# Kernel tuning notes

Measured on AMD Instinct MI355X. Metric: run time of the kernel, lower is better.

Reference implementation:

```python
import jax, jax.numpy as jnp
import numpy as np

S, B, I, H = 2048, 64, 128, 128
E = float(np.e)


def setup_inputs() -> dict:
    key = jax.random.key(0)
    ks = jax.random.split(key, 16)
    s = 1.0 / np.sqrt(H)
    inp = {
        "x": jax.random.normal(ks[0], (S, B, I), jnp.float32),
        "h0": jnp.zeros((2, B, H), jnp.float32),
        "c0": jnp.zeros((2, B, H), jnp.float32),
        # elapsed times, strictly positive
        "delta_ts": jax.random.uniform(ks[1], (B, S), jnp.float32, 0.1, 10.0),
    }
    names = ["W_ih", "W_hh", "b_ih", "b_hh", "W_d", "b_d"]
    shapes = [(4 * H, I), (4 * H, H), (4 * H,), (4 * H,), (H, H), (H,)]
    idx = 2
    for d in ["f", "r"]:
        for n, sh in zip(names, shapes):
            inp[f"{n}_{d}"] = jax.random.uniform(ks[idx], sh, jnp.float32, -s, s)
            idx += 1
    return inp


def _run_dir(x, dt, h, c, W_ih, W_hh, b_ih, b_hh, W_d, b_d):
    """Scan a TLSTM cell over time. x: [S,B,I], dt: [S,B]."""
    def step(carry, inp):
        h, c = carry
        xt, dtt = inp
        # time-aware memory decomposition (Baytas et al.)
        c_s = jnp.tanh(c @ W_d.T + b_d)               # short-term memory
        c_adj = c - c_s + c_s / jnp.log(E + dtt[:, None])  # discounted by elapsed time
        gates = xt @ W_ih.T + b_ih + h @ W_hh.T + b_hh
        i_g, f_g, g_g, o_g = jnp.split(gates, 4, axis=-1)
        c_n = jax.nn.sigmoid(f_g) * c_adj + jax.nn.sigmoid(i_g) * jnp.tanh(g_g)
        h_n = jax.nn.sigmoid(o_g) * jnp.tanh(c_n)
        return (h_n, c_n), h_n

    (h, c), ys = jax.lax.scan(step, (h, c), (x, dt))
    return ys, h, c


def reference(x, h0, c0, delta_ts,
              W_ih_f, W_hh_f, b_ih_f, b_hh_f, W_d_f, b_d_f,
              W_ih_r, W_hh_r, b_ih_r, b_hh_r, W_d_r, b_d_r):
    dt = delta_ts.T  # [S, B]
    out_f, _, _ = _run_dir(x, dt, h0[0], c0[0],
                           W_ih_f, W_hh_f, b_ih_f, b_hh_f, W_d_f, b_d_f)
    out_r, _, _ = _run_dir(x[::-1], dt[::-1], h0[1], c0[1],
                           W_ih_r, W_hh_r, b_ih_r, b_hh_r, W_d_r, b_d_r)
    return jnp.concatenate([out_f, out_r[::-1]], axis=-1)  # [S, B, 2H]
```

## Files before the change

kernel.cpp:

```cpp
#include <hip/hip_runtime.h>
#include <hip/hip_bf16.h>

#define SEQ  2048
#define BAT  64
#define HID  128
#define LDSP 136

#define XB_OFF  (1u << 20)
#define IL_OFF  (35u << 20)

typedef __bf16 bf16x8 __attribute__((ext_vector_type(8)));
typedef float  f32x4  __attribute__((ext_vector_type(4)));

#define MFMA(a,b,c) __builtin_amdgcn_mfma_f32_16x16x32_bf16((a),(b),(c),0,0,0)

__device__ __forceinline__ float sig_f(float x) {
    return __fdividef(1.0f, 1.0f + __expf(-x));
}
__device__ __forceinline__ float tanh_f(float x) {
    return 1.0f - __fdividef(2.0f, 1.0f + __expf(2.0f * x));
}
__device__ __forceinline__ bf16x8 cvt8(const float* p) {
    bf16x8 r;
    #pragma unroll
    for (int i = 0; i < 8; ++i) r[i] = (__bf16)p[i];
    return r;
}

__global__ void cvt_x_kernel(const float* __restrict__ x, __bf16* __restrict__ xb) {
    const int i = (blockIdx.x * 256 + threadIdx.x) * 4;
    const float4 v = *reinterpret_cast<const float4*>(x + i);
    __bf16 o[4];
    o[0] = (__bf16)v.x; o[1] = (__bf16)v.y; o[2] = (__bf16)v.z; o[3] = (__bf16)v.w;
    *reinterpret_cast<uint2*>(xb + i) = *reinterpret_cast<const uint2*>(o);
}

__global__ void prep_ilog_kernel(const float* __restrict__ dts, float* __restrict__ il) {
    const int idx = blockIdx.x * 256 + threadIdx.x;
    const int b = idx >> 11, t = idx & 2047;
    const float l = __logf(2.718281828459045f + dts[idx]);
    il[t * BAT + b] = __fdividef(1.0f, l) - 1.0f;
}

__global__ __launch_bounds__(512, 2) void tlstm_main(
    const __bf16* __restrict__ xb,   const float* __restrict__ ilg,
    const float* __restrict__ h0,    const float* __restrict__ c0,
    const float* __restrict__ Wih_f, const float* __restrict__ Whh_f,
    const float* __restrict__ bih_f, const float* __restrict__ bhh_f,
    const float* __restrict__ Wd_f,  const float* __restrict__ bd_f,
    const float* __restrict__ Wih_r, const float* __restrict__ Whh_r,
    const float* __restrict__ bih_r, const float* __restrict__ bhh_r,
    const float* __restrict__ Wd_r,  const float* __restrict__ bd_r,
    float* __restrict__ out)
{
    const int d    = blockIdx.x >> 4;
    const int b0   = (blockIdx.x & 15) * 4;
    const int tid  = threadIdx.x;
    const int w    = tid >> 6;
    const int lane = tid & 63;
    const int nl   = lane & 15;
    const int q    = lane >> 4;
    const int j    = w * 16 + nl;

    const float* Wih = d ? Wih_r : Wih_f;
    const float* Whh = d ? Whh_r : Whh_f;
    const float* bih = d ? bih_r : bih_f;
    const float* bhh = d ? bhh_r : bhh_f;
    const float* Wd  = d ? Wd_r  : Wd_f;
    const float* bd  = d ? bd_r  : bd_f;

    __shared__ __align__(16) __bf16 hc_a[2][16][LDSP];

    bf16x8 whh_fr[4][4], wih_fr[4][4], wd_fr[4];
    #pragma unroll
    for (int g = 0; g < 4; ++g) {
        const int row = g * 128 + j;
        #pragma unroll
        for (int kt = 0; kt < 4; ++kt) {
            const int off = row * HID + kt * 32 + q * 8;
            wih_fr[g][kt] = cvt8(Wih + off);
            whh_fr[g][kt] = cvt8(Whh + off);
        }
    }
    #pragma unroll
    for (int kt = 0; kt < 4; ++kt)
        wd_fr[kt] = cvt8(Wd + j * HID + kt * 32 + q * 8);

    float bias_g[4];
    #pragma unroll
    for (int g = 0; g < 4; ++g)
        bias_g[g] = bih[g * 128 + j] + bhh[g * 128 + j];
    const float bias_d = bd[j];
    const f32x4 bdv = f32x4{bias_d, bias_d, bias_d, bias_d};

    for (int e = tid; e < 4 * HID; e += 512) {
        const int ci = e >> 7, k = e & 127;
        hc_a[0][ci * 4][k]     = (__bf16)h0[(d * BAT + b0 + ci) * HID + k];
        hc_a[0][ci * 4 + 2][k] = (__bf16)c0[(d * BAT + b0 + ci) * HID + k];
    }
    float c_st = c0[(d * BAT + b0 + q) * HID + j];
    __syncthreads();

    const int t0      = d ? (SEQ - 1) : 0;
    const int tstep   = d ? -1 : 1;
    const int xstride = tstep * BAT * HID;
    const int istride = tstep * BAT;
    const int ostride = tstep * BAT * 256;

    const __bf16* xp0 = xb + (size_t)((t0 + tstep * (nl & 3)) * BAT + b0 + (nl >> 2)) * HID + q * 8;
    const float*  ip0 = ilg + (size_t)t0 * BAT + b0 + q;
    float*        op  = out + (size_t)(t0 * BAT + b0 + q) * 256 + d * 128 + j;

    bf16x8 xfrA[4], xfrB[4];
    float  ilA[4], ilB[4];

    #pragma unroll
    for (int kt = 0; kt < 4; ++kt) {
        xfrA[kt] = *reinterpret_cast<const bf16x8*>(xp0 + kt * 32);
        xfrB[kt] = *reinterpret_cast<const bf16x8*>(xp0 + 4 * xstride + kt * 32);
    }
    #pragma unroll
    for (int dtv = 0; dtv < 4; ++dtv) {
        ilA[dtv] = ip0[dtv * istride];
        ilB[dtv] = ip0[(4 + dtv) * istride];
    }
    const __bf16* xpl = xp0 + 8 * xstride;
    const float*  ipl = ip0 + 8 * istride;

    auto chunk = [&](bf16x8 (&xfrCur)[4], float (&ilCur)[4]) __attribute__((always_inline)) {
        f32x4 xacc[4];
        #pragma unroll
        for (int g = 0; g < 4; ++g) {
            const f32x4 bg = f32x4{bias_g[g], bias_g[g], bias_g[g], bias_g[g]};
            xacc[g] = MFMA(xfrCur[0], wih_fr[g][0], bg);
        }
        #pragma unroll
        for (int kt = 1; kt < 4; ++kt) {
            xacc[0] = MFMA(xfrCur[kt], wih_fr[0][kt], xacc[0]);
            xacc[1] = MFMA(xfrCur[kt], wih_fr[1][kt], xacc[1]);
            xacc[2] = MFMA(xfrCur[kt], wih_fr[2][kt], xacc[2]);
            xacc[3] = MFMA(xfrCur[kt], wih_fr[3][kt], xacc[3]);
        }

        #pragma unroll
        for (int dt = 0; dt < 4; ++dt) {
            const int p  = dt & 1;
            const int pn = p ^ 1;
            const int hr = dt;
            const int cr = (dt + 2) & 3;

            const float il_use = ilCur[dt];

            bf16x8 hcfr[4];
            #pragma unroll
            for (int kt = 0; kt < 4; ++kt)
                hcfr[kt] = *reinterpret_cast<const bf16x8*>(&hc_a[p][nl][kt * 32 + q * 8]);

            f32x4 ai = xacc[0], af = xacc[1], ag = xacc[2], ao = xacc[3];
            f32x4 acs = bdv;
            #pragma unroll
            for (int kt = 0; kt < 4; ++kt) {
                ai  = MFMA(hcfr[kt], whh_fr[0][kt], ai);
                af  = MFMA(hcfr[kt], whh_fr[1][kt], af);
                ag  = MFMA(hcfr[kt], whh_fr[2][kt], ag);
                ao  = MFMA(hcfr[kt], whh_fr[3][kt], ao);
                acs = MFMA(hcfr[kt], wd_fr[kt], acs);
            }

            xfrCur[dt] = *reinterpret_cast<const bf16x8*>(xpl + dt * 32);
            ilCur[dt]  = ipl[dt * istride];

            {
                const float cs   = tanh_f(acs[cr]);
                const float cadj = fmaf(cs, il_use, c_st);
                const float gi   = sig_f(ai[hr]);
                const float gf   = sig_f(af[hr]);
                const float gg   = tanh_f(ag[hr]);
                const float go   = sig_f(ao[hr]);
                const float cn   = gf * cadj + gi * gg;
                const float hn   = go * tanh_f(cn);
                c_st = cn;
                hc_a[pn][q * 4 + ((dt + 1) & 3)][j] = (__bf16)hn;
                hc_a[pn][q * 4 + ((dt + 3) & 3)][j] = (__bf16)cn;
                *op = hn;
            }
            op += ostride;

            asm volatile("s_waitcnt lgkmcnt(0)\n\ts_barrier" ::: "memory");
        }
        xpl += 4 * xstride;
        ipl += 4 * istride;
    };

    for (int tc = 0; tc < SEQ / 4; tc += 2) {
        chunk(xfrA, ilA);
        chunk(xfrB, ilB);
    }
}

extern "C" void kernel_launch(void* const* d_in, const int* in_sizes, int n_in,
                              void* d_out, int out_size, void* d_ws, size_t ws_size,
                              hipStream_t stream) {
    const float* x     = (const float*)d_in[0];
    const float* h0    = (const float*)d_in[1];
    const float* c0    = (const float*)d_in[2];
    const float* dts   = (const float*)d_in[3];
    const float* Wih_f = (const float*)d_in[4];
    const float* Whh_f = (const float*)d_in[5];
    const float* bih_f = (const float*)d_in[6];
    const float* bhh_f = (const float*)d_in[7];
    const float* Wd_f  = (const float*)d_in[8];
    const float* bd_f  = (const float*)d_in[9];
    const float* Wih_r = (const float*)d_in[10];
    const float* Whh_r = (const float*)d_in[11];
    const float* bih_r = (const float*)d_in[12];
    const float* bhh_r = (const float*)d_in[13];
    const float* Wd_r  = (const float*)d_in[14];
    const float* bd_r  = (const float*)d_in[15];
    float* out = (float*)d_out;

    __bf16* xbuf = (__bf16*)((char*)d_ws + XB_OFF);
    float*  il   = (float*)((char*)d_ws + IL_OFF);

    cvt_x_kernel<<<16384, 256, 0, stream>>>(x, xbuf);
    prep_ilog_kernel<<<512, 256, 0, stream>>>(dts, il);

    tlstm_main<<<32, 512, 0, stream>>>(xbuf, il, h0, c0,
                                       Wih_f, Whh_f, bih_f, bhh_f, Wd_f, bd_f,
                                       Wih_r, Whh_r, bih_r, bhh_r, Wd_r, bd_r,
                                       out);
}
```

Measured before the change: 1.829 ms.

## Process eight batch rows per block with two-step input tiles

Each block now handles 8 batch rows instead of 4, so the grid shrinks from 32 to 16 blocks. The 16-row MFMA tile is repacked to hold h and c for 8 rows, and the x-projection covers 2 timesteps per MFMA, where it used to cover 4. Each wave now computes two cells per step, which doubles MFMA utilisation per recurrent step while halving the number of parallel blocks. Bias adds move out of the MFMA accumulator init into the scalar epilogue. Per-step latency may rise because each thread now does more elementwise work.

```diff
diff --git a/kernel.cpp b/kernel.cpp
--- a/kernel.cpp
+++ b/kernel.cpp
@@ -53,8 +53,8 @@
     const float* __restrict__ Wd_r,  const float* __restrict__ bd_r,
     float* __restrict__ out)
 {
-    const int d    = blockIdx.x >> 4;
-    const int b0   = (blockIdx.x & 15) * 4;
+    const int d    = blockIdx.x >> 3;
+    const int b0   = (blockIdx.x & 7) * 8;
     const int tid  = threadIdx.x;
     const int w    = tid >> 6;
     const int lane = tid & 63;
@@ -69,7 +69,7 @@
     const float* Wd  = d ? Wd_r  : Wd_f;
     const float* bd  = d ? bd_r  : bd_f;
 
-    __shared__ __align__(16) __bf16 hc_a[2][16][LDSP];
+    __shared__ __align__(16) __bf16 hc[2][16][LDSP];
 
     bf16x8 whh_fr[4][4], wih_fr[4][4], wd_fr[4];
     #pragma unroll
@@ -86,19 +86,20 @@
     for (int kt = 0; kt < 4; ++kt)
         wd_fr[kt] = cvt8(Wd + j * HID + kt * 32 + q * 8);
 
-    float bias_g[4];
-    #pragma unroll
-    for (int g = 0; g < 4; ++g)
-        bias_g[g] = bih[g * 128 + j] + bhh[g * 128 + j];
-    const float bias_d = bd[j];
-    const f32x4 bdv = f32x4{bias_d, bias_d, bias_d, bias_d};
-
-    for (int e = tid; e < 4 * HID; e += 512) {
+    const float bg0 = bih[0 * 128 + j] + bhh[0 * 128 + j];
+    const float bg1 = bih[1 * 128 + j] + bhh[1 * 128 + j];
+    const float bg2 = bih[2 * 128 + j] + bhh[2 * 128 + j];
+    const float bg3 = bih[3 * 128 + j] + bhh[3 * 128 + j];
+    const float bd_s = bd[j];
+    const f32x4 zc = f32x4{0.0f, 0.0f, 0.0f, 0.0f};
+
+    for (int e = tid; e < 8 * HID; e += 512) {
         const int ci = e >> 7, k = e & 127;
-        hc_a[0][ci * 4][k]     = (__bf16)h0[(d * BAT + b0 + ci) * HID + k];
-        hc_a[0][ci * 4 + 2][k] = (__bf16)c0[(d * BAT + b0 + ci) * HID + k];
+        hc[0][2 * ci][k]     = (__bf16)h0[(d * BAT + b0 + ci) * HID + k];
+        hc[0][2 * ci + 1][k] = (__bf16)c0[(d * BAT + b0 + ci) * HID + k];
     }
-    float c_st = c0[(d * BAT + b0 + q) * HID + j];
+    float c_s0 = c0[(d * BAT + b0 + 2 * q) * HID + j];
+    float c_s1 = c0[(d * BAT + b0 + 2 * q + 1) * HID + j];
     __syncthreads();
 
     const int t0      = d ? (SEQ - 1) : 0;
@@ -107,94 +108,150 @@
     const int istride = tstep * BAT;
     const int ostride = tstep * BAT * 256;
 
-    const __bf16* xp0 = xb + (size_t)((t0 + tstep * (nl & 3)) * BAT + b0 + (nl >> 2)) * HID + q * 8;
-    const float*  ip0 = ilg + (size_t)t0 * BAT + b0 + q;
-    float*        op  = out + (size_t)(t0 * BAT + b0 + q) * 256 + d * 128 + j;
-
-    bf16x8 xfrA[4], xfrB[4];
-    float  ilA[4], ilB[4];
-
-    #pragma unroll
-    for (int kt = 0; kt < 4; ++kt) {
-        xfrA[kt] = *reinterpret_cast<const bf16x8*>(xp0 + kt * 32);
-        xfrB[kt] = *reinterpret_cast<const bf16x8*>(xp0 + 4 * xstride + kt * 32);
-    }
-    #pragma unroll
-    for (int dtv = 0; dtv < 4; ++dtv) {
-        ilA[dtv] = ip0[dtv * istride];
-        ilB[dtv] = ip0[(4 + dtv) * istride];
-    }
-    const __bf16* xpl = xp0 + 8 * xstride;
-    const float*  ipl = ip0 + 8 * istride;
-
-    auto chunk = [&](bf16x8 (&xfrCur)[4], float (&ilCur)[4]) __attribute__((always_inline)) {
-        f32x4 xacc[4];
-        #pragma unroll
-        for (int g = 0; g < 4; ++g) {
-            const f32x4 bg = f32x4{bias_g[g], bias_g[g], bias_g[g], bias_g[g]};
-            xacc[g] = MFMA(xfrCur[0], wih_fr[g][0], bg);
-        }
-        #pragma unroll
-        for (int kt = 1; kt < 4; ++kt) {
-            xacc[0] = MFMA(xfrCur[kt], wih_fr[0][kt], xacc[0]);
-            xacc[1] = MFMA(xfrCur[kt], wih_fr[1][kt], xacc[1]);
-            xacc[2] = MFMA(xfrCur[kt], wih_fr[2][kt], xacc[2]);
-            xacc[3] = MFMA(xfrCur[kt], wih_fr[3][kt], xacc[3]);
-        }
-
-        #pragma unroll
-        for (int dt = 0; dt < 4; ++dt) {
-            const int p  = dt & 1;
-            const int pn = p ^ 1;
-            const int hr = dt;
-            const int cr = (dt + 2) & 3;
-
-            const float il_use = ilCur[dt];
-
+    const __bf16* xp0 = xb + (size_t)((t0 + tstep * (nl & 1)) * BAT + b0 + (nl >> 1)) * HID + q * 8;
+    const float*  ip0 = ilg + (size_t)t0 * BAT + b0 + 2 * q;
+    float*        op  = out + (size_t)(t0 * BAT + b0 + 2 * q) * 256 + d * 128 + j;
+
+    bf16x8 xfr[4];
+    #pragma unroll
+    for (int kt = 0; kt < 4; ++kt)
+        xfr[kt] = *reinterpret_cast<const bf16x8*>(xp0 + kt * 32);
+    const __bf16* xpn = xp0 + 2 * xstride;
+
+    float2 ilP[2], ilQ[2];
+    ilP[0] = *reinterpret_cast<const float2*>(ip0);
+    ilP[1] = *reinterpret_cast<const float2*>(ip0 + istride);
+    const float* ipn = ip0 + 2 * istride;
+
+    auto pair = [&](float2 (&ilc)[2], float2 (&iln)[2]) __attribute__((always_inline)) {
+        f32x4 xa0, xa1, xa2, xa3;
+        {
             bf16x8 hcfr[4];
             #pragma unroll
             for (int kt = 0; kt < 4; ++kt)
-                hcfr[kt] = *reinterpret_cast<const bf16x8*>(&hc_a[p][nl][kt * 32 + q * 8]);
-
-            f32x4 ai = xacc[0], af = xacc[1], ag = xacc[2], ao = xacc[3];
-            f32x4 acs = bdv;
-            #pragma unroll
-            for (int kt = 0; kt < 4; ++kt) {
-                ai  = MFMA(hcfr[kt], whh_fr[0][kt], ai);
-                af  = MFMA(hcfr[kt], whh_fr[1][kt], af);
-                ag  = MFMA(hcfr[kt], whh_fr[2][kt], ag);
-                ao  = MFMA(hcfr[kt], whh_fr[3][kt], ao);
-                acs = MFMA(hcfr[kt], wd_fr[kt], acs);
-            }
-
-            xfrCur[dt] = *reinterpret_cast<const bf16x8*>(xpl + dt * 32);
-            ilCur[dt]  = ipl[dt * istride];
-
-            {
-                const float cs   = tanh_f(acs[cr]);
-                const float cadj = fmaf(cs, il_use, c_st);
-                const float gi   = sig_f(ai[hr]);
-                const float gf   = sig_f(af[hr]);
-                const float gg   = tanh_f(ag[hr]);
-                const float go   = sig_f(ao[hr]);
-                const float cn   = gf * cadj + gi * gg;
-                const float hn   = go * tanh_f(cn);
-                c_st = cn;
-                hc_a[pn][q * 4 + ((dt + 1) & 3)][j] = (__bf16)hn;
-                hc_a[pn][q * 4 + ((dt + 3) & 3)][j] = (__bf16)cn;
-                *op = hn;
+                hcfr[kt] = *reinterpret_cast<const bf16x8*>(&hc[0][nl][kt * 32 + q * 8]);
+
+            xa0 = MFMA(xfr[0], wih_fr[0][0], zc);
+            xa1 = MFMA(xfr[0], wih_fr[1][0], zc);
+            xa2 = MFMA(xfr[0], wih_fr[2][0], zc);
+            xa3 = MFMA(xfr[0], wih_fr[3][0], zc);
+            #pragma unroll
+            for (int kt = 1; kt < 4; ++kt) {
+                xa0 = MFMA(xfr[kt], wih_fr[0][kt], xa0);
+                xa1 = MFMA(xfr[kt], wih_fr[1][kt], xa1);
+                xa2 = MFMA(xfr[kt], wih_fr[2][kt], xa2);
+                xa3 = MFMA(xfr[kt], wih_fr[3][kt], xa3);
+            }
+
+            f32x4 cA = MFMA(hcfr[0], wd_fr[0],     zc);
+            f32x4 g0 = MFMA(hcfr[0], whh_fr[0][0], xa0);
+            f32x4 g1 = MFMA(hcfr[0], whh_fr[1][0], xa1);
+            f32x4 g2 = MFMA(hcfr[0], whh_fr[2][0], xa2);
+            f32x4 g3 = MFMA(hcfr[0], whh_fr[3][0], xa3);
+            #pragma unroll
+            for (int kt = 1; kt < 4; ++kt) {
+                cA = MFMA(hcfr[kt], wd_fr[kt],     cA);
+                g0 = MFMA(hcfr[kt], whh_fr[0][kt], g0);
+                g1 = MFMA(hcfr[kt], whh_fr[1][kt], g1);
+                g2 = MFMA(hcfr[kt], whh_fr[2][kt], g2);
+                g3 = MFMA(hcfr[kt], whh_fr[3][kt], g3);
+            }
+
+            {
+                const float cs   = tanh_f(cA[1] + bd_s);
+                const float cadj = fmaf(cs, ilc[0].x, c_s0);
+                const float gi   = sig_f(g0[0] + bg0);
+                const float gf   = sig_f(g1[0] + bg1);
+                const float gg   = tanh_f(g2[0] + bg2);
+                const float cn   = gf * cadj + gi * gg;
+                hc[1][4 * q + 0][j] = (__bf16)cn;
+                const float go   = sig_f(g3[0] + bg3);
+                const float hn   = go * tanh_f(cn);
+                c_s0 = cn;
+                hc[1][4 * q + 1][j] = (__bf16)hn;
+                op[0] = hn;
+            }
+            {
+                const float cs   = tanh_f(cA[3] + bd_s);
+                const float cadj = fmaf(cs, ilc[0].y, c_s1);
+                const float gi   = sig_f(g0[2] + bg0);
+                const float gf   = sig_f(g1[2] + bg1);
+                const float gg   = tanh_f(g2[2] + bg2);
+                const float cn   = gf * cadj + gi * gg;
+                hc[1][4 * q + 2][j] = (__bf16)cn;
+                const float go   = sig_f(g3[2] + bg3);
+                const float hn   = go * tanh_f(cn);
+                c_s1 = cn;
+                hc[1][4 * q + 3][j] = (__bf16)hn;
+                op[256] = hn;
             }
             op += ostride;
-
             asm volatile("s_waitcnt lgkmcnt(0)\n\ts_barrier" ::: "memory");
         }
-        xpl += 4 * xstride;
-        ipl += 4 * istride;
+        {
+            bf16x8 hcfr[4];
+            #pragma unroll
+            for (int kt = 0; kt < 4; ++kt)
+                hcfr[kt] = *reinterpret_cast<const bf16x8*>(&hc[1][nl][kt * 32 + q * 8]);
+
+            #pragma unroll
+            for (int kt = 0; kt < 4; ++kt)
+                xfr[kt] = *reinterpret_cast<const bf16x8*>(xpn + kt * 32);
+            xpn += 2 * xstride;
+            iln[0] = *reinterpret_cast<const float2*>(ipn);
+            iln[1] = *reinterpret_cast<const float2*>(ipn + istride);
+            ipn += 2 * istride;
+
+            f32x4 cA = MFMA(hcfr[0], wd_fr[0],     zc);
+            f32x4 g0 = MFMA(hcfr[0], whh_fr[0][0], xa0);
+            f32x4 g1 = MFMA(hcfr[0], whh_fr[1][0], xa1);
+            f32x4 g2 = MFMA(hcfr[0], whh_fr[2][0], xa2);
+            f32x4 g3 = MFMA(hcfr[0], whh_fr[3][0], xa3);
+            #pragma unroll
+            for (int kt = 1; kt < 4; ++kt) {
+                cA = MFMA(hcfr[kt], wd_fr[kt],     cA);
+                g0 = MFMA(hcfr[kt], whh_fr[0][kt], g0);
+                g1 = MFMA(hcfr[kt], whh_fr[1][kt], g1);
+                g2 = MFMA(hcfr[kt], whh_fr[2][kt], g2);
+                g3 = MFMA(hcfr[kt], whh_fr[3][kt], g3);
+            }
+
+            {
+                const float cs   = tanh_f(cA[0] + bd_s);
+                const float cadj = fmaf(cs, ilc[1].x, c_s0);
+                const float gi   = sig_f(g0[1] + bg0);
+                const float gf   = sig_f(g1[1] + bg1);
+                const float gg   = tanh_f(g2[1] + bg2);
+                const float cn   = gf * cadj + gi * gg;
+                hc[0][4 * q + 1][j] = (__bf16)cn;
+                const float go   = sig_f(g3[1] + bg3);
+                const float hn   = go * tanh_f(cn);
+                c_s0 = cn;
+                hc[0][4 * q + 0][j] = (__bf16)hn;
+                op[0] = hn;
+            }
+            {
+                const float cs   = tanh_f(cA[2] + bd_s);
+                const float cadj = fmaf(cs, ilc[1].y, c_s1);
+                const float gi   = sig_f(g0[3] + bg0);
+                const float gf   = sig_f(g1[3] + bg1);
+                const float gg   = tanh_f(g2[3] + bg2);
+                const float cn   = gf * cadj + gi * gg;
+                hc[0][4 * q + 3][j] = (__bf16)cn;
+                const float go   = sig_f(g3[3] + bg3);
+                const float hn   = go * tanh_f(cn);
+                c_s1 = cn;
+                hc[0][4 * q + 2][j] = (__bf16)hn;
+                op[256] = hn;
+            }
+            op += ostride;
+            asm volatile("s_waitcnt lgkmcnt(0)\n\ts_barrier" ::: "memory");
+        }
     };
 
-    for (int tc = 0; tc < SEQ / 4; tc += 2) {
-        chunk(xfrA, ilA);
-        chunk(xfrB, ilB);
+    for (int ts = 0; ts < SEQ; ts += 4) {
+        pair(ilP, ilQ);
+        pair(ilQ, ilP);
     }
 }
 
@@ -225,7 +282,7 @@
     cvt_x_kernel<<<16384, 256, 0, stream>>>(x, xbuf);
     prep_ilog_kernel<<<512, 256, 0, stream>>>(dts, il);
 
-    tlstm_main<<<32, 512, 0, stream>>>(xbuf, il, h0, c0,
+    tlstm_main<<<16, 512, 0, stream>>>(xbuf, il, h0, c0,
                                        Wih_f, Whh_f, bih_f, bhh_f, Wd_f, bd_f,
                                        Wih_r, Whh_r, bih_r, bhh_r, Wd_r, bd_r,
                                        out);
```

Measured after the change: 2.587 ms. 41.4% more time.

## Offload input projection to producer warps feeding recurrent warps via LDS

Applied to the files above, without the earlier changes.

Adds four producer wavefronts per block that compute the x·W_ih input projection (weights pre-converted to bf16 in a new kernel and streamed from global memory) one timestep ahead and publish the gate pre-activations through a shared-memory ring buffer. The eight recurrent wavefronts now only run the h/c MFMAs and the elementwise gate math, so the input GEMM is taken off the serial critical path. The trade-off is a larger block (768 threads) that shares the same barrier, extra LDS traffic for the staged pre-activations, and weight refetches from cache on every step.

```diff
diff --git a/kernel.cpp b/kernel.cpp
--- a/kernel.cpp
+++ b/kernel.cpp
@@ -8,6 +8,7 @@
 
 #define XB_OFF  (1u << 20)
 #define IL_OFF  (35u << 20)
+#define WB_OFF  ((35u << 20) + (512u << 10))
 
 typedef __bf16 bf16x8 __attribute__((ext_vector_type(8)));
 typedef float  f32x4  __attribute__((ext_vector_type(4)));
@@ -42,64 +43,38 @@
     il[t * BAT + b] = __fdividef(1.0f, l) - 1.0f;
 }
 
-__global__ __launch_bounds__(512, 2) void tlstm_main(
-    const __bf16* __restrict__ xb,   const float* __restrict__ ilg,
+__global__ void cvt_w_kernel(const float* __restrict__ Wf, const float* __restrict__ Wr,
+                             __bf16* __restrict__ wb) {
+    const int i = (blockIdx.x * 256 + threadIdx.x) * 4;
+    const int half = 512 * HID;
+    const float* src = (i < half) ? Wf : Wr;
+    const int off = (i < half) ? i : (i - half);
+    const float4 v = *reinterpret_cast<const float4*>(src + off);
+    __bf16 o[4];
+    o[0] = (__bf16)v.x; o[1] = (__bf16)v.y; o[2] = (__bf16)v.z; o[3] = (__bf16)v.w;
+    *reinterpret_cast<uint2*>(wb + i) = *reinterpret_cast<const uint2*>(o);
+}
+
+__global__ __launch_bounds__(768, 3) void tlstm_main(
+    const __bf16* __restrict__ xb,   const __bf16* __restrict__ wihb,
+    const float* __restrict__ ilg,
     const float* __restrict__ h0,    const float* __restrict__ c0,
-    const float* __restrict__ Wih_f, const float* __restrict__ Whh_f,
+    const float* __restrict__ Whh_f, const float* __restrict__ Wd_f, const float* __restrict__ bd_f,
     const float* __restrict__ bih_f, const float* __restrict__ bhh_f,
-    const float* __restrict__ Wd_f,  const float* __restrict__ bd_f,
-    const float* __restrict__ Wih_r, const float* __restrict__ Whh_r,
+    const float* __restrict__ Whh_r, const float* __restrict__ Wd_r, const float* __restrict__ bd_r,
     const float* __restrict__ bih_r, const float* __restrict__ bhh_r,
-    const float* __restrict__ Wd_r,  const float* __restrict__ bd_r,
     float* __restrict__ out)
 {
     const int d    = blockIdx.x >> 4;
     const int b0   = (blockIdx.x & 15) * 4;
     const int tid  = threadIdx.x;
-    const int w    = tid >> 6;
+    const int wv   = tid >> 6;
     const int lane = tid & 63;
     const int nl   = lane & 15;
     const int q    = lane >> 4;
-    const int j    = w * 16 + nl;
-
-    const float* Wih = d ? Wih_r : Wih_f;
-    const float* Whh = d ? Whh_r : Whh_f;
-    const float* bih = d ? bih_r : bih_f;
-    const float* bhh = d ? bhh_r : bhh_f;
-    const float* Wd  = d ? Wd_r  : Wd_f;
-    const float* bd  = d ? bd_r  : bd_f;
 
     __shared__ __align__(16) __bf16 hc_a[2][16][LDSP];
-
-    bf16x8 whh_fr[4][4], wih_fr[4][4], wd_fr[4];
-    #pragma unroll
-    for (int g = 0; g < 4; ++g) {
-        const int row = g * 128 + j;
-        #pragma unroll
-        for (int kt = 0; kt < 4; ++kt) {
-            const int off = row * HID + kt * 32 + q * 8;
-            wih_fr[g][kt] = cvt8(Wih + off);
-            whh_fr[g][kt] = cvt8(Whh + off);
-        }
-    }
-    #pragma unroll
-    for (int kt = 0; kt < 4; ++kt)
-        wd_fr[kt] = cvt8(Wd + j * HID + kt * 32 + q * 8);
-
-    float bias_g[4];
-    #pragma unroll
-    for (int g = 0; g < 4; ++g)
-        bias_g[g] = bih[g * 128 + j] + bhh[g * 128 + j];
-    const float bias_d = bd[j];
-    const f32x4 bdv = f32x4{bias_d, bias_d, bias_d, bias_d};
-
-    for (int e = tid; e < 4 * HID; e += 512) {
-        const int ci = e >> 7, k = e & 127;
-        hc_a[0][ci * 4][k]     = (__bf16)h0[(d * BAT + b0 + ci) * HID + k];
-        hc_a[0][ci * 4 + 2][k] = (__bf16)c0[(d * BAT + b0 + ci) * HID + k];
-    }
-    float c_st = c0[(d * BAT + b0 + q) * HID + j];
-    __syncthreads();
+    __shared__ __align__(16) float  pa[5][4][HID][4];
 
     const int t0      = d ? (SEQ - 1) : 0;
     const int tstep   = d ? -1 : 1;
@@ -107,94 +82,200 @@
     const int istride = tstep * BAT;
     const int ostride = tstep * BAT * 256;
 
-    const __bf16* xp0 = xb + (size_t)((t0 + tstep * (nl & 3)) * BAT + b0 + (nl >> 2)) * HID + q * 8;
-    const float*  ip0 = ilg + (size_t)t0 * BAT + b0 + q;
-    float*        op  = out + (size_t)(t0 * BAT + b0 + q) * 256 + d * 128 + j;
-
-    bf16x8 xfrA[4], xfrB[4];
-    float  ilA[4], ilB[4];
-
-    #pragma unroll
-    for (int kt = 0; kt < 4; ++kt) {
-        xfrA[kt] = *reinterpret_cast<const bf16x8*>(xp0 + kt * 32);
-        xfrB[kt] = *reinterpret_cast<const bf16x8*>(xp0 + 4 * xstride + kt * 32);
-    }
-    #pragma unroll
-    for (int dtv = 0; dtv < 4; ++dtv) {
-        ilA[dtv] = ip0[dtv * istride];
-        ilB[dtv] = ip0[(4 + dtv) * istride];
-    }
-    const __bf16* xpl = xp0 + 8 * xstride;
-    const float*  ipl = ip0 + 8 * istride;
-
-    auto chunk = [&](bf16x8 (&xfrCur)[4], float (&ilCur)[4]) __attribute__((always_inline)) {
-        f32x4 xacc[4];
+    if (wv >= 8) {
+        const int p = wv - 8;
+        const float* bih = d ? bih_r : bih_f;
+        const float* bhh = d ? bhh_r : bhh_f;
+        const __bf16* wbp = wihb + (size_t)d * 512 * HID + (size_t)(p * 128 + nl) * HID + q * 8;
+
+        float bgp[8];
+        #pragma unroll
+        for (int t = 0; t < 8; ++t) {
+            const int r = p * 128 + 16 * t + nl;
+            bgp[t] = bih[r] + bhh[r];
+        }
+
+        const __bf16* xp0 = xb + (size_t)((t0 + tstep * (nl & 3)) * BAT + b0 + (nl >> 2)) * HID + q * 8;
+        bf16x8 xfr[4];
+        #pragma unroll
+        for (int kt = 0; kt < 4; ++kt)
+            xfr[kt] = *reinterpret_cast<const bf16x8*>(xp0 + kt * 32);
+
+        f32x4 acc[8];
+        #pragma unroll
+        for (int kt = 0; kt < 4; ++kt) {
+            bf16x8 wt[8];
+            #pragma unroll
+            for (int t = 0; t < 8; ++t)
+                wt[t] = *reinterpret_cast<const bf16x8*>(wbp + (16 * t) * HID + kt * 32);
+            #pragma unroll
+            for (int t = 0; t < 8; ++t) {
+                if (kt == 0) {
+                    const f32x4 bsp = f32x4{bgp[t], bgp[t], bgp[t], bgp[t]};
+                    acc[t] = MFMA(xfr[0], wt[t], bsp);
+                } else {
+                    acc[t] = MFMA(xfr[kt], wt[t], acc[t]);
+                }
+            }
+        }
+        #pragma unroll
+        for (int t = 0; t < 8; ++t) {
+            const int dim = 16 * t + nl;
+            #pragma unroll
+            for (int r = 0; r < 4; ++r)
+                pa[r][q][dim][p] = acc[t][r];
+        }
+        const __bf16* xpn = xp0 + 4 * xstride;
+        #pragma unroll
+        for (int kt = 0; kt < 4; ++kt)
+            xfr[kt] = *reinterpret_cast<const bf16x8*>(xpn + kt * 32);
+        xpn += 4 * xstride;
+
+        bf16x8 wfA[8], wfB[8];
+        #pragma unroll
+        for (int t = 0; t < 8; ++t)
+            wfA[t] = *reinterpret_cast<const bf16x8*>(wbp + (16 * t) * HID);
+
+        __syncthreads();
+
+        auto pstep = [&](int tc, int dt, bf16x8 (&cur)[8], bf16x8 (&nxt)[8])
+            __attribute__((always_inline)) {
+            if (dt == 0) {
+                #pragma unroll
+                for (int t = 0; t < 8; ++t) {
+                    const f32x4 bsp = f32x4{bgp[t], bgp[t], bgp[t], bgp[t]};
+                    acc[t] = MFMA(xfr[0], cur[t], bsp);
+                }
+            } else {
+                #pragma unroll
+                for (int t = 0; t < 8; ++t)
+                    acc[t] = MFMA(xfr[dt], cur[t], acc[t]);
+            }
+            const int ktn = (dt + 1) & 3;
+            #pragma unroll
+            for (int t = 0; t < 8; ++t)
+                nxt[t] = *reinterpret_cast<const bf16x8*>(wbp + (16 * t) * HID + ktn * 32);
+            xfr[dt] = *reinterpret_cast<const bf16x8*>(xpn + dt * 32);
+            if (dt == 3) {
+                const int s3 = 3 + ((tc + 1) & 1);
+                #pragma unroll
+                for (int t = 0; t < 8; ++t) {
+                    const int dim = 16 * t + nl;
+                    pa[0][q][dim][p]  = acc[t][0];
+                    pa[1][q][dim][p]  = acc[t][1];
+                    pa[2][q][dim][p]  = acc[t][2];
+                    pa[s3][q][dim][p] = acc[t][3];
+                }
+            }
+            asm volatile("s_waitcnt lgkmcnt(0)\n\ts_barrier" ::: "memory");
+        };
+
+        for (int tc = 0; tc < SEQ / 4; ++tc) {
+            pstep(tc, 0, wfA, wfB);
+            pstep(tc, 1, wfB, wfA);
+            pstep(tc, 2, wfA, wfB);
+            pstep(tc, 3, wfB, wfA);
+            xpn += 4 * xstride;
+        }
+    } else {
+        const int j = wv * 16 + nl;
+        const float* Whh = d ? Whh_r : Whh_f;
+        const float* Wd  = d ? Wd_r  : Wd_f;
+        const float* bd  = d ? bd_r  : bd_f;
+
+        bf16x8 whh_fr[4][4], wd_fr[4];
         #pragma unroll
         for (int g = 0; g < 4; ++g) {
-            const f32x4 bg = f32x4{bias_g[g], bias_g[g], bias_g[g], bias_g[g]};
-            xacc[g] = MFMA(xfrCur[0], wih_fr[g][0], bg);
-        }
-        #pragma unroll
-        for (int kt = 1; kt < 4; ++kt) {
-            xacc[0] = MFMA(xfrCur[kt], wih_fr[0][kt], xacc[0]);
-            xacc[1] = MFMA(xfrCur[kt], wih_fr[1][kt], xacc[1]);
-            xacc[2] = MFMA(xfrCur[kt], wih_fr[2][kt], xacc[2]);
-            xacc[3] = MFMA(xfrCur[kt], wih_fr[3][kt], xacc[3]);
-        }
-
-        #pragma unroll
-        for (int dt = 0; dt < 4; ++dt) {
-            const int p  = dt & 1;
-            const int pn = p ^ 1;
-            const int hr = dt;
-            const int cr = (dt + 2) & 3;
-
-            const float il_use = ilCur[dt];
-
-            bf16x8 hcfr[4];
+            const int row = g * 128 + j;
             #pragma unroll
             for (int kt = 0; kt < 4; ++kt)
-                hcfr[kt] = *reinterpret_cast<const bf16x8*>(&hc_a[p][nl][kt * 32 + q * 8]);
-
-            f32x4 ai = xacc[0], af = xacc[1], ag = xacc[2], ao = xacc[3];
-            f32x4 acs = bdv;
-            #pragma unroll
-            for (int kt = 0; kt < 4; ++kt) {
-                ai  = MFMA(hcfr[kt], whh_fr[0][kt], ai);
-                af  = MFMA(hcfr[kt], whh_fr[1][kt], af);
-                ag  = MFMA(hcfr[kt], whh_fr[2][kt], ag);
-                ao  = MFMA(hcfr[kt], whh_fr[3][kt], ao);
-                acs = MFMA(hcfr[kt], wd_fr[kt], acs);
+                whh_fr[g][kt] = cvt8(Whh + row * HID + kt * 32 + q * 8);
+        }
+        #pragma unroll
+        for (int kt = 0; kt < 4; ++kt)
+            wd_fr[kt] = cvt8(Wd + j * HID + kt * 32 + q * 8);
+
+        const float bias_d = bd[j];
+        const f32x4 bdv = f32x4{bias_d, bias_d, bias_d, bias_d};
+        const f32x4 zc  = f32x4{0.0f, 0.0f, 0.0f, 0.0f};
+
+        {
+            const int ci = tid >> 7, k = tid & 127;
+            hc_a[0][ci * 4][k]     = (__bf16)h0[(d * BAT + b0 + ci) * HID + k];
+            hc_a[0][ci * 4 + 2][k] = (__bf16)c0[(d * BAT + b0 + ci) * HID + k];
+        }
+        float c_st = c0[(d * BAT + b0 + q) * HID + j];
+
+        const float* ip0 = ilg + (size_t)t0 * BAT + b0 + q;
+        float*       op  = out + (size_t)(t0 * BAT + b0 + q) * 256 + d * 128 + j;
+
+        float ilA[4], ilB[4];
+        #pragma unroll
+        for (int dtv = 0; dtv < 4; ++dtv) {
+            ilA[dtv] = ip0[dtv * istride];
+            ilB[dtv] = ip0[(4 + dtv) * istride];
+        }
+        const float* ipl = ip0 + 8 * istride;
+
+        __syncthreads();
+
+        auto echunk = [&](int tc, float (&ilCur)[4]) __attribute__((always_inline)) {
+            #pragma unroll
+            for (int dt = 0; dt < 4; ++dt) {
+                const int pp = dt & 1;
+                const int pn = pp ^ 1;
+                const int hr = dt;
+                const int cr = (dt + 2) & 3;
+                const float il_use = ilCur[dt];
+
+                bf16x8 hcfr[4];
+                #pragma unroll
+                for (int kt = 0; kt < 4; ++kt)
+                    hcfr[kt] = *reinterpret_cast<const bf16x8*>(&hc_a[pp][nl][kt * 32 + q * 8]);
+                const int ps = (dt < 3) ? dt : (3 + (tc & 1));
+                const f32x4 pav = *reinterpret_cast<const f32x4*>(&pa[ps][q][j][0]);
+
+                ilCur[dt] = ipl[dt * istride];
+
+                f32x4 cA = MFMA(hcfr[0], wd_fr[0],     bdv);
+                f32x4 g0 = MFMA(hcfr[0], whh_fr[0][0], zc);
+                f32x4 g1 = MFMA(hcfr[0], whh_fr[1][0], zc);
+                f32x4 g2 = MFMA(hcfr[0], whh_fr[2][0], zc);
+                f32x4 g3 = MFMA(hcfr[0], whh_fr[3][0], zc);
+                #pragma unroll
+                for (int kt = 1; kt < 4; ++kt) {
+                    cA = MFMA(hcfr[kt], wd_fr[kt],     cA);
+                    g0 = MFMA(hcfr[kt], whh_fr[0][kt], g0);
+                    g1 = MFMA(hcfr[kt], whh_fr[1][kt], g1);
+                    g2 = MFMA(hcfr[kt], whh_fr[2][kt], g2);
+                    g3 = MFMA(hcfr[kt], whh_fr[3][kt], g3);
+                }
+
+                {
+                    const float cs   = tanh_f(cA[cr]);
+                    const float cadj = fmaf(cs, il_use, c_st);
+                    const float gf   = sig_f(g1[hr] + pav[1]);
+                    const float gi   = sig_f(g0[hr] + pav[0]);
+                    const float gg   = tanh_f(g2[hr] + pav[2]);
+                    const float cn   = gf * cadj + gi * gg;
+                    hc_a[pn][q * 4 + ((dt + 3) & 3)][j] = (__bf16)cn;
+                    const float go   = sig_f(g3[hr] + pav[3]);
+                    const float hn   = go * tanh_f(cn);
+                    c_st = cn;
+                    hc_a[pn][q * 4 + ((dt + 1) & 3)][j] = (__bf16)hn;
+                    *op = hn;
+                }
+                op += ostride;
+
+                asm volatile("s_waitcnt lgkmcnt(0)\n\ts_barrier" ::: "memory");
             }
-
-            xfrCur[dt] = *reinterpret_cast<const bf16x8*>(xpl + dt * 32);
-            ilCur[dt]  = ipl[dt * istride];
-
-            {
-                const float cs   = tanh_f(acs[cr]);
-                const float cadj = fmaf(cs, il_use, c_st);
-                const float gi   = sig_f(ai[hr]);
-                const float gf   = sig_f(af[hr]);
-                const float gg   = tanh_f(ag[hr]);
-                const float go   = sig_f(ao[hr]);
-                const float cn   = gf * cadj + gi * gg;
-                const float hn   = go * tanh_f(cn);
-                c_st = cn;
-                hc_a[pn][q * 4 + ((dt + 1) & 3)][j] = (__bf16)hn;
-                hc_a[pn][q * 4 + ((dt + 3) & 3)][j] = (__bf16)cn;
-                *op = hn;
-            }
-            op += ostride;
-
-            asm volatile("s_waitcnt lgkmcnt(0)\n\ts_barrier" ::: "memory");
-        }
-        xpl += 4 * xstride;
-        ipl += 4 * istride;
-    };
-
-    for (int tc = 0; tc < SEQ / 4; tc += 2) {
-        chunk(xfrA, ilA);
-        chunk(xfrB, ilB);
+            ipl += 4 * istride;
+        };
+
+        for (int tc = 0; tc < SEQ / 4; tc += 2) {
+            echunk(tc,     ilA);
+            echunk(tc + 1, ilB);
+        }
     }
 }
 
@@ -221,12 +302,14 @@
 
     __bf16* xbuf = (__bf16*)((char*)d_ws + XB_OFF);
     float*  il   = (float*)((char*)d_ws + IL_OFF);
+    __bf16* wb   = (__bf16*)((char*)d_ws + WB_OFF);
 
     cvt_x_kernel<<<16384, 256, 0, stream>>>(x, xbuf);
     prep_ilog_kernel<<<512, 256, 0, stream>>>(dts, il);
-
-    tlstm_main<<<32, 512, 0, stream>>>(xbuf, il, h0, c0,
-                                       Wih_f, Whh_f, bih_f, bhh_f, Wd_f, bd_f,
-                                       Wih_r, Whh_r, bih_r, bhh_r, Wd_r, bd_r,
+    cvt_w_kernel<<<128, 256, 0, stream>>>(Wih_f, Wih_r, wb);
+
+    tlstm_main<<<32, 768, 0, stream>>>(xbuf, wb, il, h0, c0,
+                                       Whh_f, Wd_f, bd_f, bih_f, bhh_f,
+                                       Whh_r, Wd_r, bd_r, bih_r, bhh_r,
                                        out);
 }
```

Result: slower. 2.170 ms (+18.6%).
